# Performance work log

Hardware: AMD Instinct MI355X
Metric: run time of the kernel (lower is better)

The kernel has to match this reference:

```python
import jax, jax.numpy as jnp
import numpy as np

N_HASHES = 4
CHUNK = 144
REDUCTION = 4
RES_SCALE = 1.0
NORM_EPS = 5e-5


def conv2d(x, w, b, pad):
    y = jax.lax.conv_general_dilated(
        x, w, window_strides=(1, 1), padding=[(pad, pad), (pad, pad)],
        dimension_numbers=('NCHW', 'OIHW', 'NCHW'))
    return y + b[None, :, None, None]


def add_adjacent_buckets(x):
    # x: (N, h, n_chunks, chunk, e); concat each chunk with its circular neighbors
    back = jnp.roll(x, 1, axis=2)
    fwd = jnp.roll(x, -1, axis=2)
    return jnp.concatenate([x, back, fwd], axis=3)


def setup_inputs() -> dict:
    key = jax.random.key(0)
    ks = jax.random.split(key, 6)
    x = jax.random.normal(ks[0], (1, 32, 192, 192), jnp.float32)
    w_match = jax.random.normal(ks[1], (8, 32, 3, 3), jnp.float32) * 0.05
    b_match = jnp.zeros((8,), jnp.float32)
    w_asm = jax.random.normal(ks[2], (32, 32, 1, 1), jnp.float32) * 0.05
    b_asm = jnp.zeros((32,), jnp.float32)
    rotations = jax.random.normal(ks[3], (8, N_HASHES, 64), jnp.float32)
    return {'x': x, 'w_match': w_match, 'b_match': b_match,
            'w_asm': w_asm, 'b_asm': b_asm, 'rotations': rotations}


def reference(x, w_match, b_match, w_asm, b_asm, rotations):
    N, _, H, W = x.shape
    L = H * W
    # conv_match: 3x3 conv 32->8; conv_assembly: 1x1 conv 32->32
    x_embed = conv2d(x, w_match, b_match, 1).reshape(N, -1, L).transpose(0, 2, 1)  # (N, L, 8)
    y_embed = conv2d(x, w_asm, b_asm, 0).reshape(N, -1, L).transpose(0, 2, 1)      # (N, L, 32)
    C = x_embed.shape[-1]
    hash_buckets = min(L // CHUNK + (L // CHUNK) % 2, 128)  # = 128 here

    # --- LSH hashing (non-differentiable; rotations passed in for determinism) ---
    rotated = jnp.einsum('blf,fhi->bhli', x_embed, rotations)        # (N, h, L, hb/2)
    rotated = jnp.concatenate([rotated, -rotated], axis=-1)          # (N, h, L, hb)
    hash_codes = jnp.argmax(rotated, axis=-1)                        # (N, h, L)
    hash_codes = hash_codes + (jnp.arange(N_HASHES) * hash_buckets)[None, :, None]
    hash_codes = hash_codes.reshape(N, -1)                           # (N, h*L)

    # --- sort tokens by bucket id ---
    indices = jnp.argsort(hash_codes, axis=-1)
    undo_sort = jnp.argsort(indices, axis=-1)
    mod_indices = indices % L
    x_sorted = jnp.take_along_axis(x_embed, mod_indices[:, :, None], axis=1)  # (N, h*L, 8)
    y_sorted = jnp.take_along_axis(y_embed, mod_indices[:, :, None], axis=1)  # (N, h*L, 32)

    x_b = x_sorted.reshape(N, N_HASHES, -1, C)
    y_b = y_sorted.reshape(N, N_HASHES, -1, C * REDUCTION)
    padding = (-L) % CHUNK  # static; 0 for L=192*192
    if padding:
        x_b = jnp.concatenate([x_b, x_b[:, :, -padding:, :]], axis=2)
        y_b = jnp.concatenate([y_b, y_b[:, :, -padding:, :]], axis=2)
    x_b = x_b.reshape(N, N_HASHES, -1, CHUNK, C)
    y_b = y_b.reshape(N, N_HASHES, -1, CHUNK, C * REDUCTION)

    # --- bucketed attention with adjacent buckets ---
    nrm = jnp.linalg.norm(x_b, axis=-1, keepdims=True)
    x_match = x_b / jnp.maximum(nrm, NORM_EPS)   # F.normalize(eps=5e-5)
    x_match = add_adjacent_buckets(x_match)      # (N, h, k, 3*chunk, 8)
    y_adj = add_adjacent_buckets(y_b)            # (N, h, k, 3*chunk, 32)

    raw = jnp.einsum('bhkie,bhkje->bhkij', x_b, x_match)  # (N, h, k, 144, 432)
    bucket_score = jax.scipy.special.logsumexp(raw, axis=-1, keepdims=True)
    score = jnp.exp(raw - bucket_score)
    ret = jnp.einsum('bhkij,bhkje->bhkie', score, y_adj)  # (N, h, k, 144, 32)

    ret = ret.reshape(N, N_HASHES, -1, C * REDUCTION)
    bucket_score = bucket_score.reshape(N, N_HASHES, -1)
    if padding:
        ret = ret[:, :, :-padding, :]
        bucket_score = bucket_score[:, :, :-padding]
    ret = ret.reshape(N, -1, C * REDUCTION)
    bucket_score = bucket_score.reshape(N, -1)

    # --- unsort and combine hash rounds via softmax over logsumexp scores ---
    ret = jnp.take_along_axis(ret, undo_sort[:, :, None], axis=1)
    bucket_score = jnp.take_along_axis(bucket_score, undo_sort, axis=1)
    ret = ret.reshape(N, N_HASHES, L, C * REDUCTION)
    probs = jax.nn.softmax(bucket_score.reshape(N, N_HASHES, L, 1), axis=1)
    out = jnp.sum(ret * probs, axis=1)                     # (N, L, 32)
    out = out.transpose(0, 2, 1).reshape(N, -1, H, W) * RES_SCALE + x
    return out
```

## Files before the change

### kernel.cpp

```cpp
#include <hip/hip_runtime.h>
#include <hip/hip_bf16.h>
#include <math.h>

#define LTOT 36864
#define NH 4
#define NCHUNK 256
#define CHU 144
#define NBUCK 128
#define NSEG 144
#define HW_ 192
#define VTS 148

typedef unsigned int u32;
typedef unsigned short u16;
typedef unsigned long long u64;
typedef __attribute__((ext_vector_type(4))) short short4v;
typedef __attribute__((ext_vector_type(4))) float f32x4;

__device__ __forceinline__ u32 pkbf(float a, float b){
  union { __hip_bfloat162 h2; u32 u; } cv;
  cv.h2 = __float22bfloat162_rn(float2{a,b});
  return cv.u;
}
__device__ __forceinline__ float bflo(u32 w){ return __uint_as_float(w<<16); }
__device__ __forceinline__ float bfhi(u32 w){ return __uint_as_float(w & 0xffff0000u); }

__global__ __launch_bounds__(256) void k_conv(const float* __restrict__ x,
    const float* __restrict__ wm, const float* __restrict__ bm,
    const float* __restrict__ wa, const float* __restrict__ ba,
    const float* __restrict__ rot,
    u16* __restrict__ Ku, u16* __restrict__ Qu, u16* __restrict__ Vu,
    int* __restrict__ code, int* __restrict__ hist)
{
  __shared__ float xs[32*108];
  __shared__ float xq[64*8];
  const int t = threadIdx.x;
  const int id = blockIdx.x;
  const int bx = id % 12, by = id / 12;

  for (int idx=t; idx<3456; idx+=256){
    int ci = idx/108, rem = idx-ci*108;
    int iy = rem/18,  ix = rem-iy*18;
    int yy = by*4+iy-1, xx = bx*16+ix-1;
    float v = 0.f;
    if (yy>=0 && yy<HW_ && xx>=0 && xx<HW_) v = x[ci*LTOT + yy*HW_ + xx];
    xs[idx] = v;
  }
  __syncthreads();
  const int lane = t & 63;
  const int w  = __builtin_amdgcn_readfirstlane(t>>6);
  const int co0 = 2*w, cb = 8*w;
  const int ix = lane & 15, iy = lane >> 4;
  float a0 = bm[co0], a1 = bm[co0+1];
  float acc[8];
  #pragma unroll
  for (int co=0;co<8;co++) acc[co] = ba[cb+co];
  const float* xb  = xs + iy*18 + ix;
  const float* w0p = wm + co0*288;
  const float* w1p = w0p + 288;
  for (int ci=0; ci<32; ci++){
    const float* xp = xb + ci*108;
    float x00=xp[0],  x01=xp[1],  x02=xp[2];
    float x10=xp[18], x11=xp[19], x12=xp[20];
    float x20=xp[36], x21=xp[37], x22=xp[38];
    const float* w0 = w0p + ci*9;
    const float* w1 = w1p + ci*9;
    a0 += x00*w0[0]+x01*w0[1]+x02*w0[2]
        + x10*w0[3]+x11*w0[4]+x12*w0[5]
        + x20*w0[6]+x21*w0[7]+x22*w0[8];
    a1 += x00*w1[0]+x01*w1[1]+x02*w1[2]
        + x10*w1[3]+x11*w1[4]+x12*w1[5]
        + x20*w1[6]+x21*w1[7]+x22*w1[8];
    const float* wap = wa + cb*32 + ci;
    #pragma unroll
    for (int co=0;co<8;co++) acc[co] += x11 * wap[co*32];
  }
  const int l = (by*4+iy)*HW_ + bx*16+ix;
  *(float2*)(xq + lane*8 + co0) = float2{a0,a1};
  uint4 vv;
  vv.x = pkbf(acc[0],acc[1]); vv.y = pkbf(acc[2],acc[3]);
  vv.z = pkbf(acc[4],acc[5]); vv.w = pkbf(acc[6],acc[7]);
  *(uint4*)(Vu + (size_t)l*32 + cb) = vv;
  __syncthreads();

  if (t < 64){
    const int ly = t >> 4, lx = t & 15;
    const int lp = (by*4+ly)*HW_ + bx*16+lx;
    const float4* qp = (const float4*)(xq + t*8);
    float4 a = qp[0], b = qp[1];
    float n2 = a.x*a.x+a.y*a.y+a.z*a.z+a.w*a.w
             + b.x*b.x+b.y*b.y+b.z*b.z+b.w*b.w;
    float sc = 1.0f / fmaxf(sqrtf(n2), 5e-5f);
    uint4 kk, qq;
    kk.x = pkbf(a.x*sc,a.y*sc); kk.y = pkbf(a.z*sc,a.w*sc);
    kk.z = pkbf(b.x*sc,b.y*sc); kk.w = pkbf(b.z*sc,b.w*sc);
    qq.x = pkbf(a.x,a.y); qq.y = pkbf(a.z,a.w);
    qq.z = pkbf(b.x,b.y); qq.w = pkbf(b.z,b.w);
    *(uint4*)(Ku + (size_t)lp*8) = kk;
    *(uint4*)(Qu + (size_t)lp*8) = qq;
  }

  {
    const int h = w;
    const float4* qp = (const float4*)(xq + lane*8);
    float4 qa = qp[0], qb = qp[1];
    float best = -INFINITY; int bi = 0;
    float worst = INFINITY; int wi = 0;
    for (int i=0; i<64; i++){
      const float* rp = rot + h*64 + i;
      float v = qa.x*rp[0]    + qa.y*rp[256]  + qa.z*rp[512]  + qa.w*rp[768]
              + qb.x*rp[1024] + qb.y*rp[1280] + qb.z*rp[1536] + qb.w*rp[1792];
      if (v > best)  { best  = v; bi = i; }
      if (v < worst) { worst = v; wi = i; }
    }
    int c = (-worst > best) ? (64+wi) : bi;
    const int ly = lane >> 4, lx = lane & 15;
    const int lpix = (by*4+ly)*HW_ + bx*16+lx;
    code[h*LTOT + lpix] = c;
    atomicAdd(&hist[(h*NSEG + (lpix>>8))*NBUCK + c], 1);
  }
}

__global__ __launch_bounds__(256) void k_spos(const int* __restrict__ code,
    const int* __restrict__ hist, int* __restrict__ spos)
{
  const int h = blockIdx.y, seg = blockIdx.x, t = threadIdx.x;
  const int l = seg*256 + t;
  int c = code[h*LTOT + l];

  __shared__ int pre2[2][NBUCK], tot2[2][NBUCK];
  __shared__ int scv[NBUCK];
  __shared__ int segbase[NBUCK];
  __shared__ int wh[4][NBUCK];

  {
    const int b = t & 127, gg = t >> 7;
    int pre = 0, tt = 0;
    const int sA = gg*72;
    for (int s = sA; s < sA+72; s++){
      int v = hist[(h*NSEG+s)*NBUCK + b];
      tt += v;
      if (s < seg) pre += v;
    }
    pre2[gg][b] = pre; tot2[gg][b] = tt;
  }
  const int lane = t & 63, w = t >> 6;
  u64 mask = ~0ull;
  #pragma unroll
  for (int bit=0; bit<7; bit++){
    u64 bset = __ballot((c>>bit)&1);
    mask &= ((c>>bit)&1) ? bset : ~bset;
  }
  int rin = __popcll(mask & ((lane==0)?0ull:(~0ull >> (64-lane))));
  int cnt = __popcll(mask);
  ((int*)wh)[t] = 0; ((int*)wh)[t+256] = 0;
  __syncthreads();

  if (rin == 0) wh[w][c] = cnt;
  if (t < NBUCK){
    int tt = tot2[0][t] + tot2[1][t];
    int v = tt;
    #pragma unroll
    for (int off=1; off<64; off<<=1){
      int u = __shfl_up(v, off);
      if ((t & 63) >= off) v += u;
    }
    scv[t] = v;
  }
  __syncthreads();

  if (t < NBUCK){
    int tt = tot2[0][t] + tot2[1][t];
    int excl = scv[t] - tt + ((t >= 64) ? scv[63] : 0);
    segbase[t] = excl + pre2[0][t] + pre2[1][t];
  }
  __syncthreads();

  int r = segbase[c] + rin;
  for (int ww=0; ww<w; ww++) r += wh[ww][c];
  spos[h*LTOT + r] = l;
}

__global__ __launch_bounds__(320) void k_attn(const u16* __restrict__ Ku,
    const u16* __restrict__ Qu, const u16* __restrict__ Vu,
    const int* __restrict__ spos, u16* __restrict__ ret_u, float* __restrict__ bs_u)
{
  __shared__ __align__(16) u16 Klds[432*8];
  __shared__ __align__(16) u16 Qlds[CHU*8];
  __shared__ __align__(16) u16 VT[3][32*VTS];
  __shared__ float qn[CHU];
  __shared__ int spos_l[CHU];

  const int t = threadIdx.x;
  const int k = blockIdx.x, h = blockIdx.y;

  if (t < CHU){
    int pos0 = spos[h*LTOT + k*CHU + t];
    spos_l[t] = pos0;
    uint4 qv = *(const uint4*)(Qu + (size_t)pos0*8);
    *(uint4*)(Qlds + t*8) = qv;
    float f0=bflo(qv.x), f1=bfhi(qv.x), f2=bflo(qv.y), f3=bfhi(qv.y);
    float f4=bflo(qv.z), f5=bfhi(qv.z), f6=bflo(qv.w), f7=bfhi(qv.w);
    qn[t] = sqrtf(f0*f0+f1*f1+f2*f2+f3*f3+f4*f4+f5*f5+f6*f6+f7*f7)*1.01f + 1e-6f;
    #pragma unroll
    for (int rr=0; rr<3; rr++){
      const int gkb = ((k + NCHUNK-1 + rr) & (NCHUNK-1)) * CHU;
      int pk = spos[h*LTOT + gkb + t];
      *(uint4*)(Klds + (rr*CHU + t)*8) = *(const uint4*)(Ku + (size_t)pk*8);
    }
  }
  for (int j = t; j < 432; j += 320){
    int p = j >> 1, hf = j & 1;
    int g = 2*p;
    int rg = g / CHU, lk = g - rg*CHU;
    const int gkb = ((k + NCHUNK-1 + rg) & (NCHUNK-1)) * CHU;
    int posA = spos[h*LTOT + gkb + lk];
    int posB = spos[h*LTOT + gkb + lk + 1];
    const uint4* ra = (const uint4*)(Vu + (size_t)posA*32);
    const uint4* rb = (const uint4*)(Vu + (size_t)posB*32);
    uint4 A0 = ra[hf*2], A1 = ra[hf*2+1];
    uint4 B0 = rb[hf*2], B1 = rb[hf*2+1];
    u32 aw[8] = {A0.x,A0.y,A0.z,A0.w,A1.x,A1.y,A1.z,A1.w};
    u32 bw[8] = {B0.x,B0.y,B0.z,B0.w,B1.x,B1.y,B1.z,B1.w};
    int ebase = hf*16;
    u16* vtb = (u16*)VT[rg];
    #pragma unroll
    for (int m=0;m<8;m++){
      u32 al = aw[m]&0xffffu, ah = aw[m]>>16;
      u32 bl = bw[m]&0xffffu, bh = bw[m]>>16;
      *(u32*)&vtb[(ebase+2*m  )*VTS + lk] = al | (bl<<16);
      *(u32*)&vtb[(ebase+2*m+1)*VTS + lk] = ah | (bh<<16);
    }
  }
  __syncthreads();

  const int lane = t & 63;
  const int wv = t >> 6;
  const int q = lane & 15;
  const int quad = lane >> 4;
  const bool two = (wv < 4);
  const int tl0 = 2*wv;
  const int tl1 = two ? (2*wv+1) : 8;

  const short4v zs = {0,0,0,0};
  short4v bq0 = zs, bq1 = zs;
  if (quad < 2){
    bq0 = *(const short4v*)(Qlds + (tl0*16+q)*8 + quad*4);
    if (two) bq1 = *(const short4v*)(Qlds + (tl1*16+q)*8 + quad*4);
  }
  const float m0 = qn[tl0*16+q];
  const float m1 = two ? qn[tl1*16+q] : 0.f;

  f32x4 o00={0,0,0,0}, o01={0,0,0,0}, o10={0,0,0,0}, o11={0,0,0,0};
  float s0 = 0.f, s1 = 0.f;

  #pragma unroll 3
  for (int kt=0; kt<27; kt++){
    const int rg = kt / 9, ktl = kt - rg*9;
    const u16* vtb = VT[rg];
    short4v av = zs;
    if (quad < 2) av = *(const short4v*)(Klds + (kt*16+q)*8 + quad*4);
    f32x4 zc = {0.f,0.f,0.f,0.f};
    f32x4 stA = __builtin_amdgcn_mfma_f32_16x16x16bf16_1k(av, bq0, zc, 0,0,0);

    float pA0 = __expf(stA[0]-m0), pA1 = __expf(stA[1]-m0);
    float pA2 = __expf(stA[2]-m0), pA3 = __expf(stA[3]-m0);
    s0 += (pA0+pA1)+(pA2+pA3);
    union { u32 u[2]; short4v s4; } pkA;
    pkA.u[0] = pkbf(pA0,pA1); pkA.u[1] = pkbf(pA2,pA3);

    short4v va0 = *(const short4v*)(&vtb[ q    *VTS + ktl*16 + quad*4]);
    short4v va1 = *(const short4v*)(&vtb[(q+16)*VTS + ktl*16 + quad*4]);
    o00 = __builtin_amdgcn_mfma_f32_16x16x16bf16_1k(va0, pkA.s4, o00, 0,0,0);
    o01 = __builtin_amdgcn_mfma_f32_16x16x16bf16_1k(va1, pkA.s4, o01, 0,0,0);

    if (two){
      f32x4 stB = __builtin_amdgcn_mfma_f32_16x16x16bf16_1k(av, bq1, zc, 0,0,0);
      float pB0 = __expf(stB[0]-m1), pB1 = __expf(stB[1]-m1);
      float pB2 = __expf(stB[2]-m1), pB3 = __expf(stB[3]-m1);
      s1 += (pB0+pB1)+(pB2+pB3);
      union { u32 u[2]; short4v s4; } pkB;
      pkB.u[0] = pkbf(pB0,pB1); pkB.u[1] = pkbf(pB2,pB3);
      o10 = __builtin_amdgcn_mfma_f32_16x16x16bf16_1k(va0, pkB.s4, o10, 0,0,0);
      o11 = __builtin_amdgcn_mfma_f32_16x16x16bf16_1k(va1, pkB.s4, o11, 0,0,0);
    }
  }

  float st0 = s0;
  st0 += __shfl_xor(st0, 16); st0 += __shfl_xor(st0, 32);
  float inv0 = 1.0f/st0;

  const int pos0 = spos_l[tl0*16 + q];
  u16* rp0 = ret_u + (size_t)(h*LTOT + pos0)*32;
  uint2 wA, wB;
  wA.x = pkbf(o00[0]*inv0, o00[1]*inv0); wA.y = pkbf(o00[2]*inv0, o00[3]*inv0);
  wB.x = pkbf(o01[0]*inv0, o01[1]*inv0); wB.y = pkbf(o01[2]*inv0, o01[3]*inv0);
  *(uint2*)&rp0[quad*4]    = wA;
  *(uint2*)&rp0[16+quad*4] = wB;
  if (quad == 0) bs_u[h*LTOT + pos0] = m0 + __logf(st0);

  if (two){
    float st1 = s1;
    st1 += __shfl_xor(st1, 16); st1 += __shfl_xor(st1, 32);
    float inv1 = 1.0f/st1;
    const int pos1 = spos_l[tl1*16 + q];
    u16* rp1 = ret_u + (size_t)(h*LTOT + pos1)*32;
    wA.x = pkbf(o10[0]*inv1, o10[1]*inv1); wA.y = pkbf(o10[2]*inv1, o10[3]*inv1);
    wB.x = pkbf(o11[0]*inv1, o11[1]*inv1); wB.y = pkbf(o11[2]*inv1, o11[3]*inv1);
    *(uint2*)&rp1[quad*4]    = wA;
    *(uint2*)&rp1[16+quad*4] = wB;
    if (quad == 0) bs_u[h*LTOT + pos1] = m1 + __logf(st1);
  }
}

__global__ __launch_bounds__(256) void k_final(const float* __restrict__ x,
    const u16* __restrict__ ret_u, const float* __restrict__ bs_u,
    float* __restrict__ out)
{
  const int l  = blockIdx.x*64 + (threadIdx.x & 63);
  const int eg = threadIdx.x >> 6;
  float bs[NH];
  #pragma unroll
  for (int h=0;h<NH;h++) bs[h] = bs_u[h*LTOT + l];
  float m = fmaxf(fmaxf(bs[0],bs[1]), fmaxf(bs[2],bs[3]));
  float p[NH]; float s = 0.f;
  #pragma unroll
  for (int h=0;h<NH;h++){ p[h] = __expf(bs[h]-m); s += p[h]; }
  float inv = 1.0f/s;
  float o[8];
  #pragma unroll
  for (int e=0;e<8;e++) o[e]=0.f;
  #pragma unroll
  for (int h=0;h<NH;h++){
    float w = p[h]*inv;
    uint4 v = *(const uint4*)(ret_u + (size_t)(h*LTOT + l)*32 + eg*8);
    o[0] += w*bflo(v.x); o[1] += w*bfhi(v.x);
    o[2] += w*bflo(v.y); o[3] += w*bfhi(v.y);
    o[4] += w*bflo(v.z); o[5] += w*bfhi(v.z);
    o[6] += w*bflo(v.w); o[7] += w*bfhi(v.w);
  }
  #pragma unroll
  for (int e=0;e<8;e++){
    int ge = eg*8 + e;
    out[ge*LTOT + l] = o[e] + x[ge*LTOT + l];
  }
}

extern "C" void kernel_launch(void* const* d_in, const int* in_sizes, int n_in,
                              void* d_out, int out_size, void* d_ws, size_t ws_size,
                              hipStream_t stream)
{
  const float* x   = (const float*)d_in[0];
  const float* wm  = (const float*)d_in[1];
  const float* bm  = (const float*)d_in[2];
  const float* wa  = (const float*)d_in[3];
  const float* ba  = (const float*)d_in[4];
  const float* rot = (const float*)d_in[5];
  float* out = (float*)d_out;

  char* ws = (char*)d_ws;
  size_t off = 0;
  auto alloc = [&](size_t bytes)->void*{
    void* p = ws + off;
    off = (off + bytes + 255) & ~(size_t)255;
    return p;
  };
  u16*   Ku     = (u16*)  alloc((size_t)LTOT*8*2);
  u16*   Qu     = (u16*)  alloc((size_t)LTOT*8*2);
  u16*   Vu     = (u16*)  alloc((size_t)LTOT*32*2);
  int*   code   = (int*)  alloc((size_t)NH*LTOT*4);
  int*   hist   = (int*)  alloc((size_t)NH*NSEG*NBUCK*4);
  int*   spos   = (int*)  alloc((size_t)NH*LTOT*4);
  u16*   ret_u  = (u16*)  alloc((size_t)NH*LTOT*32*2);
  float* bs_u   = (float*)alloc((size_t)NH*LTOT*4);

  hipMemsetAsync(hist, 0, (size_t)NH*NSEG*NBUCK*4, stream);
  hipLaunchKernelGGL(k_conv,   dim3(576),        dim3(256), 0, stream, x, wm, bm, wa, ba, rot, Ku, Qu, Vu, code, hist);
  hipLaunchKernelGGL(k_spos,   dim3(NSEG,NH),    dim3(256), 0, stream, code, hist, spos);
  hipLaunchKernelGGL(k_attn,   dim3(NCHUNK,NH),  dim3(320), 0, stream, Ku, Qu, Vu, spos, ret_u, bs_u);
  hipLaunchKernelGGL(k_final,  dim3(576),        dim3(256), 0, stream, x, ret_u, bs_u, out);
}
```

Before: 127.4 us.

## Fuse all stages into one persistent cooperative kernel with grid syncs

Replaces the memset and four separate kernel launches with a single cooperative persistent kernel. Grid-wide barriers separate the phases, and shared memory is overlaid through a union. Blocks are sized to 320 threads everywhere, which idles 64 threads in the conv, spos and final phases. The aim is to remove launch gaps and the memset, at the cost of grid.sync overhead, lower occupancy from the larger union LDS footprint, and serialized loops when blocks are fewer than work units. A fallback multi-kernel path handles cooperative launch failure.

```diff
diff --git a/kernel.cpp b/kernel.cpp
--- a/kernel.cpp
+++ b/kernel.cpp
@@ -1,6 +1,9 @@
 #include <hip/hip_runtime.h>
 #include <hip/hip_bf16.h>
+#include <hip/hip_cooperative_groups.h>
 #include <math.h>
+
+namespace cg = cooperative_groups;
 
 #define LTOT 36864
 #define NH 4
@@ -25,20 +28,31 @@
 __device__ __forceinline__ float bflo(u32 w){ return __uint_as_float(w<<16); }
 __device__ __forceinline__ float bfhi(u32 w){ return __uint_as_float(w & 0xffff0000u); }
 
-__global__ __launch_bounds__(256) void k_conv(const float* __restrict__ x,
+union __align__(16) SMu {
+  struct { float xs[32*108]; float xq[64*8]; } c;
+  struct { u16 Klds[432*8]; u16 Qlds[CHU*8]; u16 VT[3][32*VTS];
+           float qn[CHU]; int spos_l[CHU]; } a;
+  struct { int pre2[2][NBUCK]; int tot2[2][NBUCK]; int scv[NBUCK];
+           int segbase[NBUCK]; int wh[4][NBUCK]; } s;
+};
+
+__device__ __forceinline__ void phase_zero(int gid, int gsize, int* __restrict__ hist){
+  for (int i = gid; i < NH*NSEG*NBUCK; i += gsize) hist[i] = 0;
+}
+
+__device__ __forceinline__ void phase_conv(const float* __restrict__ x,
     const float* __restrict__ wm, const float* __restrict__ bm,
     const float* __restrict__ wa, const float* __restrict__ ba,
     const float* __restrict__ rot,
     u16* __restrict__ Ku, u16* __restrict__ Qu, u16* __restrict__ Vu,
-    int* __restrict__ code, int* __restrict__ hist)
-{
-  __shared__ float xs[32*108];
-  __shared__ float xq[64*8];
-  const int t = threadIdx.x;
-  const int id = blockIdx.x;
+    int* __restrict__ code, int* __restrict__ hist,
+    int id, int t, SMu& sm)
+{
+  float* xs = sm.c.xs;
+  float* xq = sm.c.xq;
   const int bx = id % 12, by = id / 12;
 
-  for (int idx=t; idx<3456; idx+=256){
+  for (int idx=t; idx<3456; idx+=320){
     int ci = idx/108, rem = idx-ci*108;
     int iy = rem/18,  ix = rem-iy*18;
     int yy = by*4+iy-1, xx = bx*16+ix-1;
@@ -48,39 +62,41 @@
   }
   __syncthreads();
   const int lane = t & 63;
-  const int w  = __builtin_amdgcn_readfirstlane(t>>6);
-  const int co0 = 2*w, cb = 8*w;
-  const int ix = lane & 15, iy = lane >> 4;
-  float a0 = bm[co0], a1 = bm[co0+1];
-  float acc[8];
-  #pragma unroll
-  for (int co=0;co<8;co++) acc[co] = ba[cb+co];
-  const float* xb  = xs + iy*18 + ix;
-  const float* w0p = wm + co0*288;
-  const float* w1p = w0p + 288;
-  for (int ci=0; ci<32; ci++){
-    const float* xp = xb + ci*108;
-    float x00=xp[0],  x01=xp[1],  x02=xp[2];
-    float x10=xp[18], x11=xp[19], x12=xp[20];
-    float x20=xp[36], x21=xp[37], x22=xp[38];
-    const float* w0 = w0p + ci*9;
-    const float* w1 = w1p + ci*9;
-    a0 += x00*w0[0]+x01*w0[1]+x02*w0[2]
-        + x10*w0[3]+x11*w0[4]+x12*w0[5]
-        + x20*w0[6]+x21*w0[7]+x22*w0[8];
-    a1 += x00*w1[0]+x01*w1[1]+x02*w1[2]
-        + x10*w1[3]+x11*w1[4]+x12*w1[5]
-        + x20*w1[6]+x21*w1[7]+x22*w1[8];
-    const float* wap = wa + cb*32 + ci;
+  if (t < 256){
+    const int w  = __builtin_amdgcn_readfirstlane(t>>6);
+    const int co0 = 2*w, cb = 8*w;
+    const int ix = lane & 15, iy = lane >> 4;
+    float a0 = bm[co0], a1 = bm[co0+1];
+    float acc[8];
     #pragma unroll
-    for (int co=0;co<8;co++) acc[co] += x11 * wap[co*32];
-  }
-  const int l = (by*4+iy)*HW_ + bx*16+ix;
-  *(float2*)(xq + lane*8 + co0) = float2{a0,a1};
-  uint4 vv;
-  vv.x = pkbf(acc[0],acc[1]); vv.y = pkbf(acc[2],acc[3]);
-  vv.z = pkbf(acc[4],acc[5]); vv.w = pkbf(acc[6],acc[7]);
-  *(uint4*)(Vu + (size_t)l*32 + cb) = vv;
+    for (int co=0;co<8;co++) acc[co] = ba[cb+co];
+    const float* xb  = xs + iy*18 + ix;
+    const float* w0p = wm + co0*288;
+    const float* w1p = w0p + 288;
+    for (int ci=0; ci<32; ci++){
+      const float* xp = xb + ci*108;
+      float x00=xp[0],  x01=xp[1],  x02=xp[2];
+      float x10=xp[18], x11=xp[19], x12=xp[20];
+      float x20=xp[36], x21=xp[37], x22=xp[38];
+      const float* w0 = w0p + ci*9;
+      const float* w1 = w1p + ci*9;
+      a0 += x00*w0[0]+x01*w0[1]+x02*w0[2]
+          + x10*w0[3]+x11*w0[4]+x12*w0[5]
+          + x20*w0[6]+x21*w0[7]+x22*w0[8];
+      a1 += x00*w1[0]+x01*w1[1]+x02*w1[2]
+          + x10*w1[3]+x11*w1[4]+x12*w1[5]
+          + x20*w1[6]+x21*w1[7]+x22*w1[8];
+      const float* wap = wa + cb*32 + ci;
+      #pragma unroll
+      for (int co=0;co<8;co++) acc[co] += x11 * wap[co*32];
+    }
+    const int l = (by*4+iy)*HW_ + bx*16+ix;
+    *(float2*)(xq + lane*8 + co0) = float2{a0,a1};
+    uint4 vv;
+    vv.x = pkbf(acc[0],acc[1]); vv.y = pkbf(acc[2],acc[3]);
+    vv.z = pkbf(acc[4],acc[5]); vv.w = pkbf(acc[6],acc[7]);
+    *(uint4*)(Vu + (size_t)l*32 + cb) = vv;
+  }
   __syncthreads();
 
   if (t < 64){
@@ -100,8 +116,8 @@
     *(uint4*)(Qu + (size_t)lp*8) = qq;
   }
 
-  {
-    const int h = w;
+  if (t < 256){
+    const int h = __builtin_amdgcn_readfirstlane(t>>6);
     const float4* qp = (const float4*)(xq + lane*8);
     float4 qa = qp[0], qb = qp[1];
     float best = -INFINITY; int bi = 0;
@@ -119,21 +135,19 @@
     code[h*LTOT + lpix] = c;
     atomicAdd(&hist[(h*NSEG + (lpix>>8))*NBUCK + c], 1);
   }
-}
-
-__global__ __launch_bounds__(256) void k_spos(const int* __restrict__ code,
-    const int* __restrict__ hist, int* __restrict__ spos)
-{
-  const int h = blockIdx.y, seg = blockIdx.x, t = threadIdx.x;
+  __syncthreads();
+}
+
+__device__ __forceinline__ void phase_spos(const int* __restrict__ code,
+    const int* __restrict__ hist, int* __restrict__ spos,
+    int u, int t, SMu& sm)
+{
+  const int h = u / NSEG, seg = u - h*NSEG;
   const int l = seg*256 + t;
-  int c = code[h*LTOT + l];
-
-  __shared__ int pre2[2][NBUCK], tot2[2][NBUCK];
-  __shared__ int scv[NBUCK];
-  __shared__ int segbase[NBUCK];
-  __shared__ int wh[4][NBUCK];
-
-  {
+  int c = 0;
+  if (t < 256) c = code[h*LTOT + l];
+
+  if (t < 256){
     const int b = t & 127, gg = t >> 7;
     int pre = 0, tt = 0;
     const int sA = gg*72;
@@ -142,7 +156,7 @@
       tt += v;
       if (s < seg) pre += v;
     }
-    pre2[gg][b] = pre; tot2[gg][b] = tt;
+    sm.s.pre2[gg][b] = pre; sm.s.tot2[gg][b] = tt;
   }
   const int lane = t & 63, w = t >> 6;
   u64 mask = ~0ull;
@@ -153,46 +167,47 @@
   }
   int rin = __popcll(mask & ((lane==0)?0ull:(~0ull >> (64-lane))));
   int cnt = __popcll(mask);
-  ((int*)wh)[t] = 0; ((int*)wh)[t+256] = 0;
-  __syncthreads();
-
-  if (rin == 0) wh[w][c] = cnt;
+  if (t < 256){ ((int*)sm.s.wh)[t] = 0; ((int*)sm.s.wh)[t+256] = 0; }
+  __syncthreads();
+
+  if (t < 256 && rin == 0) sm.s.wh[w][c] = cnt;
   if (t < NBUCK){
-    int tt = tot2[0][t] + tot2[1][t];
+    int tt = sm.s.tot2[0][t] + sm.s.tot2[1][t];
     int v = tt;
     #pragma unroll
     for (int off=1; off<64; off<<=1){
-      int u = __shfl_up(v, off);
-      if ((t & 63) >= off) v += u;
-    }
-    scv[t] = v;
+      int uu = __shfl_up(v, off);
+      if ((t & 63) >= off) v += uu;
+    }
+    sm.s.scv[t] = v;
   }
   __syncthreads();
 
   if (t < NBUCK){
-    int tt = tot2[0][t] + tot2[1][t];
-    int excl = scv[t] - tt + ((t >= 64) ? scv[63] : 0);
-    segbase[t] = excl + pre2[0][t] + pre2[1][t];
-  }
-  __syncthreads();
-
-  int r = segbase[c] + rin;
-  for (int ww=0; ww<w; ww++) r += wh[ww][c];
-  spos[h*LTOT + r] = l;
-}
-
-__global__ __launch_bounds__(320) void k_attn(const u16* __restrict__ Ku,
+    int tt = sm.s.tot2[0][t] + sm.s.tot2[1][t];
+    int excl = sm.s.scv[t] - tt + ((t >= 64) ? sm.s.scv[63] : 0);
+    sm.s.segbase[t] = excl + sm.s.pre2[0][t] + sm.s.pre2[1][t];
+  }
+  __syncthreads();
+
+  if (t < 256){
+    int r = sm.s.segbase[c] + rin;
+    for (int ww=0; ww<w; ww++) r += sm.s.wh[ww][c];
+    spos[h*LTOT + r] = l;
+  }
+  __syncthreads();
+}
+
+__device__ __forceinline__ void phase_attn(const u16* __restrict__ Ku,
     const u16* __restrict__ Qu, const u16* __restrict__ Vu,
-    const int* __restrict__ spos, u16* __restrict__ ret_u, float* __restrict__ bs_u)
-{
-  __shared__ __align__(16) u16 Klds[432*8];
-  __shared__ __align__(16) u16 Qlds[CHU*8];
-  __shared__ __align__(16) u16 VT[3][32*VTS];
-  __shared__ float qn[CHU];
-  __shared__ int spos_l[CHU];
-
-  const int t = threadIdx.x;
-  const int k = blockIdx.x, h = blockIdx.y;
+    const int* __restrict__ spos, u16* __restrict__ ret_u, float* __restrict__ bs_u,
+    int u, int t, SMu& sm)
+{
+  const int k = u & (NCHUNK-1), h = u >> 8;
+  u16* Klds = sm.a.Klds;
+  u16* Qlds = sm.a.Qlds;
+  float* qn = sm.a.qn;
+  int* spos_l = sm.a.spos_l;
 
   if (t < CHU){
     int pos0 = spos[h*LTOT + k*CHU + t];
@@ -223,7 +238,7 @@
     u32 aw[8] = {A0.x,A0.y,A0.z,A0.w,A1.x,A1.y,A1.z,A1.w};
     u32 bw[8] = {B0.x,B0.y,B0.z,B0.w,B1.x,B1.y,B1.z,B1.w};
     int ebase = hf*16;
-    u16* vtb = (u16*)VT[rg];
+    u16* vtb = (u16*)sm.a.VT[rg];
     #pragma unroll
     for (int m=0;m<8;m++){
       u32 al = aw[m]&0xffffu, ah = aw[m]>>16;
@@ -257,7 +272,7 @@
   #pragma unroll 3
   for (int kt=0; kt<27; kt++){
     const int rg = kt / 9, ktl = kt - rg*9;
-    const u16* vtb = VT[rg];
+    const u16* vtb = sm.a.VT[rg];
     short4v av = zs;
     if (quad < 2) av = *(const short4v*)(Klds + (kt*16+q)*8 + quad*4);
     f32x4 zc = {0.f,0.f,0.f,0.f};
@@ -311,14 +326,16 @@
     *(uint2*)&rp1[16+quad*4] = wB;
     if (quad == 0) bs_u[h*LTOT + pos1] = m1 + __logf(st1);
   }
-}
-
-__global__ __launch_bounds__(256) void k_final(const float* __restrict__ x,
+  __syncthreads();
+}
+
+__device__ __forceinline__ void phase_final(const float* __restrict__ x,
     const u16* __restrict__ ret_u, const float* __restrict__ bs_u,
-    float* __restrict__ out)
-{
-  const int l  = blockIdx.x*64 + (threadIdx.x & 63);
-  const int eg = threadIdx.x >> 6;
+    float* __restrict__ out, int u, int t)
+{
+  if (t >= 256) return;
+  const int l  = u*64 + (t & 63);
+  const int eg = t >> 6;
   float bs[NH];
   #pragma unroll
   for (int h=0;h<NH;h++) bs[h] = bs_u[h*LTOT + l];
@@ -344,6 +361,65 @@
     int ge = eg*8 + e;
     out[ge*LTOT + l] = o[e] + x[ge*LTOT + l];
   }
+}
+
+__global__ __launch_bounds__(320) void k_fused(const float* __restrict__ x,
+    const float* __restrict__ wm, const float* __restrict__ bm,
+    const float* __restrict__ wa, const float* __restrict__ ba,
+    const float* __restrict__ rot,
+    u16* __restrict__ Ku, u16* __restrict__ Qu, u16* __restrict__ Vu,
+    int* __restrict__ code, int* __restrict__ hist, int* __restrict__ spos,
+    u16* __restrict__ ret_u, float* __restrict__ bs_u, float* __restrict__ out)
+{
+  __shared__ SMu sm;
+  cg::grid_group grid = cg::this_grid();
+  const int t = threadIdx.x;
+  const int bid = blockIdx.x;
+  const int nb = gridDim.x;
+
+  phase_zero(bid*320 + t, nb*320, hist);
+  grid.sync();
+  for (int u = bid; u < 576; u += nb)
+    phase_conv(x, wm, bm, wa, ba, rot, Ku, Qu, Vu, code, hist, u, t, sm);
+  grid.sync();
+  for (int u = bid; u < NH*NSEG; u += nb)
+    phase_spos(code, hist, spos, u, t, sm);
+  grid.sync();
+  for (int u = bid; u < NCHUNK*NH; u += nb)
+    phase_attn(Ku, Qu, Vu, spos, ret_u, bs_u, u, t, sm);
+  grid.sync();
+  for (int u = bid; u < 576; u += nb)
+    phase_final(x, ret_u, bs_u, out, u, t);
+}
+
+__global__ __launch_bounds__(320) void k_conv_l(const float* __restrict__ x,
+    const float* __restrict__ wm, const float* __restrict__ bm,
+    const float* __restrict__ wa, const float* __restrict__ ba,
+    const float* __restrict__ rot,
+    u16* __restrict__ Ku, u16* __restrict__ Qu, u16* __restrict__ Vu,
+    int* __restrict__ code, int* __restrict__ hist)
+{
+  __shared__ SMu sm;
+  phase_conv(x, wm, bm, wa, ba, rot, Ku, Qu, Vu, code, hist, blockIdx.x, threadIdx.x, sm);
+}
+__global__ __launch_bounds__(320) void k_spos_l(const int* __restrict__ code,
+    const int* __restrict__ hist, int* __restrict__ spos)
+{
+  __shared__ SMu sm;
+  phase_spos(code, hist, spos, blockIdx.x, threadIdx.x, sm);
+}
+__global__ __launch_bounds__(320) void k_attn_l(const u16* __restrict__ Ku,
+    const u16* __restrict__ Qu, const u16* __restrict__ Vu,
+    const int* __restrict__ spos, u16* __restrict__ ret_u, float* __restrict__ bs_u)
+{
+  __shared__ SMu sm;
+  phase_attn(Ku, Qu, Vu, spos, ret_u, bs_u, blockIdx.x, threadIdx.x, sm);
+}
+__global__ __launch_bounds__(320) void k_final_l(const float* __restrict__ x,
+    const u16* __restrict__ ret_u, const float* __restrict__ bs_u,
+    float* __restrict__ out)
+{
+  phase_final(x, ret_u, bs_u, out, blockIdx.x, threadIdx.x);
 }
 
 extern "C" void kernel_launch(void* const* d_in, const int* in_sizes, int n_in,
@@ -374,9 +450,29 @@
   u16*   ret_u  = (u16*)  alloc((size_t)NH*LTOT*32*2);
   float* bs_u   = (float*)alloc((size_t)NH*LTOT*4);
 
-  hipMemsetAsync(hist, 0, (size_t)NH*NSEG*NBUCK*4, stream);
-  hipLaunchKernelGGL(k_conv,   dim3(576),        dim3(256), 0, stream, x, wm, bm, wa, ba, rot, Ku, Qu, Vu, code, hist);
-  hipLaunchKernelGGL(k_spos,   dim3(NSEG,NH),    dim3(256), 0, stream, code, hist, spos);
-  hipLaunchKernelGGL(k_attn,   dim3(NCHUNK,NH),  dim3(320), 0, stream, Ku, Qu, Vu, spos, ret_u, bs_u);
-  hipLaunchKernelGGL(k_final,  dim3(576),        dim3(256), 0, stream, x, ret_u, bs_u, out);
-}
+  static int coop_blocks = -1;
+  if (coop_blocks < 0){
+    int occ = 0;
+    hipError_t qe = hipOccupancyMaxActiveBlocksPerMultiprocessor(&occ, (const void*)k_fused, 320, 0);
+    if (qe != hipSuccess || occ < 1) occ = 1;
+    int nb = occ * 256;
+    if (nb > NCHUNK*NH) nb = NCHUNK*NH;
+    coop_blocks = nb;
+  }
+
+  hipError_t e = hipLaunchCooperativeKernel((const void*)k_fused,
+      dim3(coop_blocks), dim3(320),
+      (void**)(void*[]){ (void*)&x, (void*)&wm, (void*)&bm, (void*)&wa, (void*)&ba, (void*)&rot,
+                         (void*)&Ku, (void*)&Qu, (void*)&Vu, (void*)&code, (void*)&hist, (void*)&spos,
+                         (void*)&ret_u, (void*)&bs_u, (void*)&out },
+      0, stream);
+
+  if (e != hipSuccess){
+    (void)hipGetLastError();
+    hipMemsetAsync(hist, 0, (size_t)NH*NSEG*NBUCK*4, stream);
+    hipLaunchKernelGGL(k_conv_l,  dim3(576),        dim3(320), 0, stream, x, wm, bm, wa, ba, rot, Ku, Qu, Vu, code, hist);
+    hipLaunchKernelGGL(k_spos_l,  dim3(NSEG*NH),    dim3(320), 0, stream, code, hist, spos);
+    hipLaunchKernelGGL(k_attn_l,  dim3(NCHUNK*NH),  dim3(320), 0, stream, Ku, Qu, Vu, spos, ret_u, bs_u);
+    hipLaunchKernelGGL(k_final_l, dim3(576),        dim3(320), 0, stream, x, ret_u, bs_u, out);
+  }
+}
```

After: 367.7 us. 2.89x slower.
